# Optimization experiments

Measured on AMD Instinct MI355X. Metric: run time of the kernel, lower is better.

The kernel has to match this reference:

```python
import jax, jax.numpy as jnp
import numpy as np

GRAPH_WEIGHT = 0.3


def setup_inputs() -> dict:
    key = jax.random.key(0)
    ks = jax.random.split(key, 6)
    B, N, NB, MAXKV, BS = 8, 1048576, 8192, 32, 128
    logits = jax.random.normal(ks[0], (B, N, 1), dtype=jnp.float32)
    targets = jax.random.bernoulli(ks[1], 0.5, (B, N)).astype(jnp.float32)
    sup_mask = jax.random.bernoulli(ks[2], 0.1, (B, N))
    ignore_mask = jax.random.bernoulli(ks[3], 0.05, (B, N))
    kv_indices = jax.random.randint(ks[4], (B, NB, MAXKV), 0, NB)
    kv_num_blocks = jax.random.randint(ks[5], (B, NB), 0, MAXKV + 1)
    return {
        "logits": logits,
        "targets": targets,
        "sup_mask": sup_mask,
        "ignore_mask": ignore_mask,
        "kv_indices": kv_indices,
        "kv_num_blocks": kv_num_blocks,
        "block_size": BS,
    }


def _loss(logits, targets, sup_mask, ignore_mask, kv_indices, kv_num_blocks, block_size):
    x = logits.squeeze(-1)                      # [B, N]
    B, N = x.shape
    nb = N // block_size
    dt = x.dtype

    # ---- supervised BCE over sup_mask (== BCEWithLogitsLoss on gathered set) ----
    per = jnp.maximum(x, 0) - x * targets + jnp.log1p(jnp.exp(-jnp.abs(x)))
    supf = sup_mask.astype(dt)
    sup_cnt = supf.sum()
    loss_sup = jnp.where(sup_cnt > 0, (per * supf).sum() / jnp.maximum(sup_cnt, 1), jnp.asarray(0, dt))

    # ---- graph smoothness (block-sparse neighbor-mean squared error) ----
    probs = jax.nn.sigmoid(x)                   # [B, N]
    uncertain = (~ignore_mask) & (~sup_mask)
    keep = (~ignore_mask).astype(dt)

    pblk = probs.reshape(B, nb, block_size)     # [B, nb, BS]
    kblk = keep.reshape(B, nb, block_size)
    block_sum = (pblk * kblk).sum(-1)           # [B, nb] sum of non-ignored probs per block
    block_cnt = kblk.sum(-1)                    # [B, nb]

    max_kv = kv_indices.shape[-1]
    flat_idx = kv_indices.reshape(B, nb * max_kv)
    g_sum = jnp.take_along_axis(block_sum, flat_idx, axis=1).reshape(B, nb, max_kv)
    g_cnt = jnp.take_along_axis(block_cnt, flat_idx, axis=1).reshape(B, nb, max_kv)
    kv_valid = (jnp.arange(max_kv)[None, None, :] < kv_num_blocks[..., None]).astype(dt)
    neigh_sum = (g_sum * kv_valid).sum(-1)      # [B, nb]
    neigh_cnt = (g_cnt * kv_valid).sum(-1)
    neigh_mean = neigh_sum / jnp.maximum(neigh_cnt, 1)

    ublk = uncertain.reshape(B, nb, block_size).astype(dt)
    q_cnt = ublk.sum(-1)                        # [B, nb] uncertain q nodes per block
    valid_block = (q_cnt > 0) & (kv_num_blocks > 0) & (neigh_cnt > 0)

    sq = (((pblk - neigh_mean[..., None]) ** 2) * ublk).sum(-1)  # [B, nb]
    vb = valid_block.astype(dt)
    loss_b = (sq * vb).sum(-1)                  # [B]
    count_b = (q_cnt * vb).sum(-1)              # [B]
    batch_valid = count_b > 0
    per_batch = jnp.where(batch_valid, loss_b / jnp.maximum(count_b, 1), 0.0)
    loss_graph = per_batch.sum() / jnp.maximum(batch_valid.sum(), 1).astype(dt)
    loss_graph = jnp.where(uncertain.any(), loss_graph, jnp.asarray(0, dt))

    return loss_sup + GRAPH_WEIGHT * loss_graph


def reference(logits, targets, sup_mask, ignore_mask, kv_indices, kv_num_blocks, block_size):
    return _loss(logits, targets, sup_mask, ignore_mask, kv_indices, kv_num_blocks, block_size)
```

## Files before the change

kernel.cpp:

```cpp
#include <hip/hip_runtime.h>

constexpr int BATCH = 8;
constexpr int NPB   = 1 << 20;
constexpr int BS    = 128;
constexpr int NB    = NPB / BS;
constexpr int NBLK  = BATCH * NB;
constexpr int MAXKV = 32;

#define GRAPH_WEIGHT 0.3f

constexpr int P1_WGS = (BATCH * NPB) / (256 * 8);
constexpr int P2_WGS = 2048;

constexpr int WS_BSC = 0;
constexpr int WS_QUP = 2 * NBLK;
constexpr int WS_SUP = WS_QUP + 4 * NBLK;
constexpr int WS_P2  = WS_SUP + 2 * P1_WGS;

typedef float v4f __attribute__((ext_vector_type(4)));
typedef int   v4i __attribute__((ext_vector_type(4)));

__global__ __launch_bounds__(256) void k_phase1(const v4f* __restrict__ lg4,
                                                const v4f* __restrict__ tg4,
                                                const v4i* __restrict__ sm4,
                                                const v4i* __restrict__ im4,
                                                float* __restrict__ ws)
{
    const int lane = threadIdx.x & 63;
    const int wid  = (blockIdx.x << 2) + (threadIdx.x >> 6);
    const int grp  = lane >> 4;
    const int sub  = lane & 15;
    const int blk  = (wid << 2) + grp;
    const int c0   = (blk << 5) + sub;

    v4f xv[2], tv[2];
    v4i sv[2], gv[2];
    xv[0] = __builtin_nontemporal_load(lg4 + c0);
    xv[1] = __builtin_nontemporal_load(lg4 + c0 + 16);
    tv[0] = __builtin_nontemporal_load(tg4 + c0);
    tv[1] = __builtin_nontemporal_load(tg4 + c0 + 16);
    sv[0] = __builtin_nontemporal_load(sm4 + c0);
    sv[1] = __builtin_nontemporal_load(sm4 + c0 + 16);
    gv[0] = __builtin_nontemporal_load(im4 + c0);
    gv[1] = __builtin_nontemporal_load(im4 + c0 + 16);

    float sup_sum = 0.f, sup_cnt = 0.f;
    float bsum = 0.f, bcnt = 0.f, q = 0.f, up = 0.f, up2 = 0.f;

#pragma unroll
    for (int j = 0; j < 2; ++j) {
#pragma unroll
        for (int k = 0; k < 4; ++k) {
            const float x = xv[j][k], t = tv[j][k];
            const bool s = (sv[j][k] != 0);
            const bool g = (gv[j][k] != 0);

            const float ax  = fabsf(x);
            const float e   = __expf(-ax);
            const float lp  = __logf(1.f + e);
            const float per = fmaxf(x, 0.f) - x * t + lp;
            const float inv = 1.f / (1.f + e);
            const float p   = (x >= 0.f) ? inv : e * inv;

            if (s) { sup_sum += per; sup_cnt += 1.f; }
            if (!g) { bsum += p; bcnt += 1.f; }
            if (!g && !s) { q += 1.f; up += p; up2 += p * p; }
        }
    }

#pragma unroll
    for (int d = 8; d >= 1; d >>= 1) {
        bsum += __shfl_xor(bsum, d);
        bcnt += __shfl_xor(bcnt, d);
        q    += __shfl_xor(q, d);
        up   += __shfl_xor(up, d);
        up2  += __shfl_xor(up2, d);
    }
    if (sub == 0) {
        *reinterpret_cast<float2*>(ws + WS_BSC + 2 * blk) = make_float2(bsum, bcnt);
        *reinterpret_cast<float4*>(ws + WS_QUP + 4 * blk) = make_float4(q, up, up2, 0.f);
    }

#pragma unroll
    for (int d = 32; d >= 1; d >>= 1) {
        sup_sum += __shfl_xor(sup_sum, d);
        sup_cnt += __shfl_xor(sup_cnt, d);
    }
    __shared__ float lsup[4][2];
    const int w = threadIdx.x >> 6;
    if (lane == 0) { lsup[w][0] = sup_sum; lsup[w][1] = sup_cnt; }
    __syncthreads();
    if (threadIdx.x == 0) {
        const float a = lsup[0][0] + lsup[1][0] + lsup[2][0] + lsup[3][0];
        const float b = lsup[0][1] + lsup[1][1] + lsup[2][1] + lsup[3][1];
        *reinterpret_cast<float2*>(ws + WS_SUP + 2 * blockIdx.x) = make_float2(a, b);
    }
}

__global__ __launch_bounds__(256) void k_phase2(const int* __restrict__ kvi,
                                                const int* __restrict__ kvn,
                                                float* __restrict__ ws)
{
    const int hw     = threadIdx.x >> 5;
    const int lane32 = threadIdx.x & 31;
    const int h0     = blockIdx.x * 32 + hw * 4;
    const int bbase  = (blockIdx.x >> 8) << 13;

    const v4i nkv4 = *reinterpret_cast<const v4i*>(kvn + h0);

    int idxs[4];
#pragma unroll
    for (int j = 0; j < 4; ++j)
        idxs[j] = __builtin_nontemporal_load(kvi + (size_t)(h0 + j) * MAXKV + lane32);

    float gsv[4], gcv[4];
#pragma unroll
    for (int j = 0; j < 4; ++j) {
        float gs = 0.f, gc = 0.f;
        if (lane32 < nkv4[j]) {
            const float2 v = *reinterpret_cast<const float2*>(ws + WS_BSC + 2 * (bbase + idxs[j]));
            gs = v.x; gc = v.y;
        }
#pragma unroll
        for (int d = 16; d >= 1; d >>= 1) {
            gs += __shfl_xor(gs, d);
            gc += __shfl_xor(gc, d);
        }
        gsv[j] = gs; gcv[j] = gc;
    }

    float L = 0.f, C = 0.f, U = 0.f;
    if (lane32 < 4) {
        const int k = lane32;
        const float4 quv = *reinterpret_cast<const float4*>(ws + WS_QUP + 4 * (h0 + k));
        const float q = quv.x, up = quv.y, up2 = quv.z;
        const float gs = gsv[k], gc = gcv[k];
        const float m  = gs / fmaxf(gc, 1.f);
        const bool  vb = (q > 0.f) && (nkv4[k] > 0) && (gc > 0.f);
        const float sq = up2 - 2.f * m * up + m * m * q;
        L = vb ? sq : 0.f;
        C = vb ? q  : 0.f;
        U = q;
    }
#pragma unroll
    for (int d = 2; d >= 1; d >>= 1) {
        L += __shfl_xor(L, d);
        C += __shfl_xor(C, d);
        U += __shfl_xor(U, d);
    }

    __shared__ float l2s[8][3];
    if (lane32 == 0) { l2s[hw][0] = L; l2s[hw][1] = C; l2s[hw][2] = U; }
    __syncthreads();
    if (threadIdx.x == 0) {
        float Ls = 0.f, Cs = 0.f, Us = 0.f;
#pragma unroll
        for (int j = 0; j < 8; ++j) { Ls += l2s[j][0]; Cs += l2s[j][1]; Us += l2s[j][2]; }
        *reinterpret_cast<float4*>(ws + WS_P2 + 4 * blockIdx.x) = make_float4(Ls, Cs, Us, 0.f);
    }
}

__global__ __launch_bounds__(512) void k_phase3(const float* __restrict__ ws,
                                                float* __restrict__ out)
{
    const int tid  = threadIdx.x;
    const int lane = tid & 63;
    const int w    = tid >> 6;

    __shared__ float lsup[8][2];
    __shared__ float lfin[8][3];

    const v4f* supf4 = reinterpret_cast<const v4f*>(ws + WS_SUP);
    float ss = 0.f, sc = 0.f;
#pragma unroll
    for (int j = 0; j < 4; ++j) {
        const v4f v = __builtin_nontemporal_load(supf4 + tid * 4 + j);
        ss += v.x + v.z; sc += v.y + v.w;
    }
#pragma unroll
    for (int d = 32; d >= 1; d >>= 1) { ss += __shfl_xor(ss, d); sc += __shfl_xor(sc, d); }
    if (lane == 0) { lsup[w][0] = ss; lsup[w][1] = sc; }

    const v4f* p2f4 = reinterpret_cast<const v4f*>(ws + WS_P2);
    float L = 0.f, C = 0.f, U = 0.f;
#pragma unroll
    for (int j = 0; j < 4; ++j) {
        const v4f v = __builtin_nontemporal_load(p2f4 + w * 256 + lane * 4 + j);
        L += v.x; C += v.y; U += v.z;
    }
#pragma unroll
    for (int d = 32; d >= 1; d >>= 1) {
        L += __shfl_xor(L, d);
        C += __shfl_xor(C, d);
        U += __shfl_xor(U, d);
    }
    if (lane == 0) { lfin[w][0] = L; lfin[w][1] = C; lfin[w][2] = U; }
    __syncthreads();

    if (tid == 0) {
        float ssum = 0.f, scn = 0.f;
#pragma unroll
        for (int j = 0; j < 8; ++j) { ssum += lsup[j][0]; scn += lsup[j][1]; }
        float per = 0.f, nv = 0.f, uc = 0.f;
#pragma unroll
        for (int b = 0; b < 8; ++b) {
            const float l = lfin[b][0], c = lfin[b][1], u = lfin[b][2];
            if (c > 0.f) { per += l / fmaxf(c, 1.f); nv += 1.f; }
            uc += u;
        }
        const float loss_sup = (scn > 0.f) ? ssum / fmaxf(scn, 1.f) : 0.f;
        float lgr = per / fmaxf(nv, 1.f);
        if (!(uc > 0.f)) lgr = 0.f;
        out[0] = loss_sup + GRAPH_WEIGHT * lgr;
    }
}

extern "C" void kernel_launch(void* const* d_in, const int* in_sizes, int n_in,
                              void* d_out, int out_size, void* d_ws, size_t ws_size,
                              hipStream_t stream) {
    const v4f* lg4 = (const v4f*)d_in[0];
    const v4f* tg4 = (const v4f*)d_in[1];
    const v4i* sm4 = (const v4i*)d_in[2];
    const v4i* im4 = (const v4i*)d_in[3];
    const int* kvi = (const int*)d_in[4];
    const int* kvn = (const int*)d_in[5];
    float* ws  = (float*)d_ws;
    float* out = (float*)d_out;

    k_phase1<<<P1_WGS, 256, 0, stream>>>(lg4, tg4, sm4, im4, ws);
    k_phase2<<<P2_WGS, 256, 0, stream>>>(kvi, kvn, ws);
    k_phase3<<<1, 512, 0, stream>>>(ws, out);
}
```

Before: 164.1 us.

## Fuse final reduction into phase2 via last-block atomic counter; widen phase1 per-thread work

Phase 1 now has each 8-lane group cover one 128-element block, with 16 elements per thread, which halves the workgroup count and shortens the shuffle reduction. The separate single-workgroup phase-3 launch is removed. Phase 2 workgroups instead bump hierarchical atomic counters, and the last one to finish performs the final reduction and writes the output. This saves one kernel launch and its dependency gap, at the cost of atomics and fences, and it relies on phase 1 zeroing the counters before phase 2 runs.

```diff
diff --git a/kernel.cpp b/kernel.cpp
--- a/kernel.cpp
+++ b/kernel.cpp
@@ -9,13 +9,14 @@
 
 #define GRAPH_WEIGHT 0.3f
 
-constexpr int P1_WGS = (BATCH * NPB) / (256 * 8);
+constexpr int P1_WGS = (BATCH * NPB) / (256 * 16);
 constexpr int P2_WGS = 2048;
 
 constexpr int WS_BSC = 0;
 constexpr int WS_QUP = 2 * NBLK;
 constexpr int WS_SUP = WS_QUP + 4 * NBLK;
 constexpr int WS_P2  = WS_SUP + 2 * P1_WGS;
+constexpr int WS_CNT = WS_P2 + 4 * P2_WGS;
 
 typedef float v4f __attribute__((ext_vector_type(4)));
 typedef int   v4i __attribute__((ext_vector_type(4)));
@@ -26,29 +27,32 @@
                                                 const v4i* __restrict__ im4,
                                                 float* __restrict__ ws)
 {
+    if (blockIdx.x == 0 && threadIdx.x < 33)
+        reinterpret_cast<unsigned*>(ws)[WS_CNT + threadIdx.x * 32] = 0u;
+
     const int lane = threadIdx.x & 63;
     const int wid  = (blockIdx.x << 2) + (threadIdx.x >> 6);
-    const int grp  = lane >> 4;
-    const int sub  = lane & 15;
-    const int blk  = (wid << 2) + grp;
+    const int grp  = lane >> 3;
+    const int sub  = lane & 7;
+    const int blk  = (wid << 3) + grp;
     const int c0   = (blk << 5) + sub;
 
-    v4f xv[2], tv[2];
-    v4i sv[2], gv[2];
-    xv[0] = __builtin_nontemporal_load(lg4 + c0);
-    xv[1] = __builtin_nontemporal_load(lg4 + c0 + 16);
-    tv[0] = __builtin_nontemporal_load(tg4 + c0);
-    tv[1] = __builtin_nontemporal_load(tg4 + c0 + 16);
-    sv[0] = __builtin_nontemporal_load(sm4 + c0);
-    sv[1] = __builtin_nontemporal_load(sm4 + c0 + 16);
-    gv[0] = __builtin_nontemporal_load(im4 + c0);
-    gv[1] = __builtin_nontemporal_load(im4 + c0 + 16);
+    v4f xv[4], tv[4];
+    v4i sv[4], gv[4];
+#pragma unroll
+    for (int j = 0; j < 4; ++j) xv[j] = __builtin_nontemporal_load(lg4 + c0 + (j << 3));
+#pragma unroll
+    for (int j = 0; j < 4; ++j) tv[j] = __builtin_nontemporal_load(tg4 + c0 + (j << 3));
+#pragma unroll
+    for (int j = 0; j < 4; ++j) sv[j] = __builtin_nontemporal_load(sm4 + c0 + (j << 3));
+#pragma unroll
+    for (int j = 0; j < 4; ++j) gv[j] = __builtin_nontemporal_load(im4 + c0 + (j << 3));
 
     float sup_sum = 0.f, sup_cnt = 0.f;
     float bsum = 0.f, bcnt = 0.f, q = 0.f, up = 0.f, up2 = 0.f;
 
 #pragma unroll
-    for (int j = 0; j < 2; ++j) {
+    for (int j = 0; j < 4; ++j) {
 #pragma unroll
         for (int k = 0; k < 4; ++k) {
             const float x = xv[j][k], t = tv[j][k];
@@ -69,7 +73,7 @@
     }
 
 #pragma unroll
-    for (int d = 8; d >= 1; d >>= 1) {
+    for (int d = 4; d >= 1; d >>= 1) {
         bsum += __shfl_xor(bsum, d);
         bcnt += __shfl_xor(bcnt, d);
         q    += __shfl_xor(q, d);
@@ -99,10 +103,12 @@
 
 __global__ __launch_bounds__(256) void k_phase2(const int* __restrict__ kvi,
                                                 const int* __restrict__ kvn,
-                                                float* __restrict__ ws)
+                                                float* __restrict__ ws,
+                                                float* __restrict__ out)
 {
-    const int hw     = threadIdx.x >> 5;
-    const int lane32 = threadIdx.x & 31;
+    const int tid    = threadIdx.x;
+    const int hw     = tid >> 5;
+    const int lane32 = tid & 31;
     const int h0     = blockIdx.x * 32 + hw * 4;
     const int bbase  = (blockIdx.x >> 8) << 13;
 
@@ -150,61 +156,74 @@
     }
 
     __shared__ float l2s[8][3];
+    __shared__ bool  is_last;
     if (lane32 == 0) { l2s[hw][0] = L; l2s[hw][1] = C; l2s[hw][2] = U; }
     __syncthreads();
-    if (threadIdx.x == 0) {
+    if (tid == 0) {
         float Ls = 0.f, Cs = 0.f, Us = 0.f;
 #pragma unroll
         for (int j = 0; j < 8; ++j) { Ls += l2s[j][0]; Cs += l2s[j][1]; Us += l2s[j][2]; }
         *reinterpret_cast<float4*>(ws + WS_P2 + 4 * blockIdx.x) = make_float4(Ls, Cs, Us, 0.f);
-    }
-}
-
-__global__ __launch_bounds__(512) void k_phase3(const float* __restrict__ ws,
-                                                float* __restrict__ out)
-{
-    const int tid  = threadIdx.x;
+
+        __threadfence();
+        unsigned* cnts = reinterpret_cast<unsigned*>(ws) + WS_CNT;
+        const unsigned prev = atomicAdd(cnts + (blockIdx.x & 31) * 32, 1u);
+        bool last = false;
+        if (prev == (P2_WGS / 32) - 1) {
+            const unsigned pm = atomicAdd(cnts + 32 * 32, 1u);
+            last = (pm == 31);
+        }
+        is_last = last;
+    }
+    __syncthreads();
+    if (!is_last) return;
+
+    __threadfence();
     const int lane = tid & 63;
     const int w    = tid >> 6;
 
-    __shared__ float lsup[8][2];
-    __shared__ float lfin[8][3];
+    __shared__ float fsup[4][2];
+    __shared__ float ffin[8][3];
 
     const v4f* supf4 = reinterpret_cast<const v4f*>(ws + WS_SUP);
     float ss = 0.f, sc = 0.f;
 #pragma unroll
     for (int j = 0; j < 4; ++j) {
-        const v4f v = __builtin_nontemporal_load(supf4 + tid * 4 + j);
+        const v4f v = supf4[tid * 4 + j];
         ss += v.x + v.z; sc += v.y + v.w;
     }
 #pragma unroll
     for (int d = 32; d >= 1; d >>= 1) { ss += __shfl_xor(ss, d); sc += __shfl_xor(sc, d); }
-    if (lane == 0) { lsup[w][0] = ss; lsup[w][1] = sc; }
+    if (lane == 0) { fsup[w][0] = ss; fsup[w][1] = sc; }
 
     const v4f* p2f4 = reinterpret_cast<const v4f*>(ws + WS_P2);
-    float L = 0.f, C = 0.f, U = 0.f;
-#pragma unroll
-    for (int j = 0; j < 4; ++j) {
-        const v4f v = __builtin_nontemporal_load(p2f4 + w * 256 + lane * 4 + j);
-        L += v.x; C += v.y; U += v.z;
-    }
-#pragma unroll
-    for (int d = 32; d >= 1; d >>= 1) {
-        L += __shfl_xor(L, d);
-        C += __shfl_xor(C, d);
-        U += __shfl_xor(U, d);
-    }
-    if (lane == 0) { lfin[w][0] = L; lfin[w][1] = C; lfin[w][2] = U; }
+#pragma unroll
+    for (int bb = 0; bb < 2; ++bb) {
+        const int b = 2 * w + bb;
+        float Lb = 0.f, Cb = 0.f, Ub = 0.f;
+#pragma unroll
+        for (int j = 0; j < 4; ++j) {
+            const v4f v = p2f4[b * 256 + lane * 4 + j];
+            Lb += v.x; Cb += v.y; Ub += v.z;
+        }
+#pragma unroll
+        for (int d = 32; d >= 1; d >>= 1) {
+            Lb += __shfl_xor(Lb, d);
+            Cb += __shfl_xor(Cb, d);
+            Ub += __shfl_xor(Ub, d);
+        }
+        if (lane == 0) { ffin[b][0] = Lb; ffin[b][1] = Cb; ffin[b][2] = Ub; }
+    }
     __syncthreads();
 
     if (tid == 0) {
         float ssum = 0.f, scn = 0.f;
 #pragma unroll
-        for (int j = 0; j < 8; ++j) { ssum += lsup[j][0]; scn += lsup[j][1]; }
+        for (int j = 0; j < 4; ++j) { ssum += fsup[j][0]; scn += fsup[j][1]; }
         float per = 0.f, nv = 0.f, uc = 0.f;
 #pragma unroll
         for (int b = 0; b < 8; ++b) {
-            const float l = lfin[b][0], c = lfin[b][1], u = lfin[b][2];
+            const float l = ffin[b][0], c = ffin[b][1], u = ffin[b][2];
             if (c > 0.f) { per += l / fmaxf(c, 1.f); nv += 1.f; }
             uc += u;
         }
@@ -228,6 +247,5 @@
     float* out = (float*)d_out;
 
     k_phase1<<<P1_WGS, 256, 0, stream>>>(lg4, tg4, sm4, im4, ws);
-    k_phase2<<<P2_WGS, 256, 0, stream>>>(kvi, kvn, ws);
-    k_phase3<<<1, 512, 0, stream>>>(ws, out);
+    k_phase2<<<P2_WGS, 256, 0, stream>>>(kvi, kvn, ws, out);
 }
```

Measured after the change: 196.7 us. +19.9%, slower.

## Make phase1 persistent with double-buffered loads over eight iterations per wave

Applied to the files above, without the earlier changes.

Phase1 drops from 4096 single-shot workgroups to 512 workgroups, each wave looping over eight groups of four blocks. The loads for the next iteration are issued before computing the current one, so memory latency overlaps with math. This cuts launch and tail overhead and reduces the number of partial sup sums phase3 must read. It also doubles register use for the buffers, which can lower occupancy, and 512 workgroups may not fully saturate HBM bandwidth.

```diff
diff --git a/kernel.cpp b/kernel.cpp
--- a/kernel.cpp
+++ b/kernel.cpp
@@ -9,8 +9,9 @@
 
 #define GRAPH_WEIGHT 0.3f
 
-constexpr int P1_WGS = (BATCH * NPB) / (256 * 8);
-constexpr int P2_WGS = 2048;
+constexpr int P1_WGS   = 512;
+constexpr int P1_ITERS = 8;
+constexpr int P2_WGS   = 2048;
 
 constexpr int WS_BSC = 0;
 constexpr int WS_QUP = 2 * NBLK;
@@ -27,58 +28,70 @@
                                                 float* __restrict__ ws)
 {
     const int lane = threadIdx.x & 63;
-    const int wid  = (blockIdx.x << 2) + (threadIdx.x >> 6);
+    const int wv   = threadIdx.x >> 6;
+    const int W    = (blockIdx.x << 2) + wv;
     const int grp  = lane >> 4;
     const int sub  = lane & 15;
-    const int blk  = (wid << 2) + grp;
-    const int c0   = (blk << 5) + sub;
-
-    v4f xv[2], tv[2];
-    v4i sv[2], gv[2];
-    xv[0] = __builtin_nontemporal_load(lg4 + c0);
-    xv[1] = __builtin_nontemporal_load(lg4 + c0 + 16);
-    tv[0] = __builtin_nontemporal_load(tg4 + c0);
-    tv[1] = __builtin_nontemporal_load(tg4 + c0 + 16);
-    sv[0] = __builtin_nontemporal_load(sm4 + c0);
-    sv[1] = __builtin_nontemporal_load(sm4 + c0 + 16);
-    gv[0] = __builtin_nontemporal_load(im4 + c0);
-    gv[1] = __builtin_nontemporal_load(im4 + c0 + 16);
+    const int cb   = (W * 32 + grp) * 32 + sub;
+
+    v4f xb[2][2], tb[2][2];
+    v4i sb[2][2], gb[2][2];
+
+    auto load_iter = [&](int buf, int it) {
+        const int c = cb + it * 128;
+        xb[buf][0] = __builtin_nontemporal_load(lg4 + c);
+        xb[buf][1] = __builtin_nontemporal_load(lg4 + c + 16);
+        tb[buf][0] = __builtin_nontemporal_load(tg4 + c);
+        tb[buf][1] = __builtin_nontemporal_load(tg4 + c + 16);
+        sb[buf][0] = __builtin_nontemporal_load(sm4 + c);
+        sb[buf][1] = __builtin_nontemporal_load(sm4 + c + 16);
+        gb[buf][0] = __builtin_nontemporal_load(im4 + c);
+        gb[buf][1] = __builtin_nontemporal_load(im4 + c + 16);
+    };
 
     float sup_sum = 0.f, sup_cnt = 0.f;
-    float bsum = 0.f, bcnt = 0.f, q = 0.f, up = 0.f, up2 = 0.f;
-
-#pragma unroll
-    for (int j = 0; j < 2; ++j) {
-#pragma unroll
-        for (int k = 0; k < 4; ++k) {
-            const float x = xv[j][k], t = tv[j][k];
-            const bool s = (sv[j][k] != 0);
-            const bool g = (gv[j][k] != 0);
-
-            const float ax  = fabsf(x);
-            const float e   = __expf(-ax);
-            const float lp  = __logf(1.f + e);
-            const float per = fmaxf(x, 0.f) - x * t + lp;
-            const float inv = 1.f / (1.f + e);
-            const float p   = (x >= 0.f) ? inv : e * inv;
-
-            if (s) { sup_sum += per; sup_cnt += 1.f; }
-            if (!g) { bsum += p; bcnt += 1.f; }
-            if (!g && !s) { q += 1.f; up += p; up2 += p * p; }
-        }
-    }
-
-#pragma unroll
-    for (int d = 8; d >= 1; d >>= 1) {
-        bsum += __shfl_xor(bsum, d);
-        bcnt += __shfl_xor(bcnt, d);
-        q    += __shfl_xor(q, d);
-        up   += __shfl_xor(up, d);
-        up2  += __shfl_xor(up2, d);
-    }
-    if (sub == 0) {
-        *reinterpret_cast<float2*>(ws + WS_BSC + 2 * blk) = make_float2(bsum, bcnt);
-        *reinterpret_cast<float4*>(ws + WS_QUP + 4 * blk) = make_float4(q, up, up2, 0.f);
+    load_iter(0, 0);
+
+#pragma unroll
+    for (int it = 0; it < P1_ITERS; ++it) {
+        if (it + 1 < P1_ITERS) load_iter((it + 1) & 1, it + 1);
+        const int buf = it & 1;
+
+        float bsum = 0.f, bcnt = 0.f, q = 0.f, up = 0.f, up2 = 0.f;
+#pragma unroll
+        for (int h = 0; h < 2; ++h) {
+#pragma unroll
+            for (int k = 0; k < 4; ++k) {
+                const float x = xb[buf][h][k], t = tb[buf][h][k];
+                const bool s = (sb[buf][h][k] != 0);
+                const bool g = (gb[buf][h][k] != 0);
+
+                const float ax  = fabsf(x);
+                const float e   = __expf(-ax);
+                const float lp  = __logf(1.f + e);
+                const float per = fmaxf(x, 0.f) - x * t + lp;
+                const float inv = 1.f / (1.f + e);
+                const float p   = (x >= 0.f) ? inv : e * inv;
+
+                if (s) { sup_sum += per; sup_cnt += 1.f; }
+                if (!g) { bsum += p; bcnt += 1.f; }
+                if (!g && !s) { q += 1.f; up += p; up2 += p * p; }
+            }
+        }
+
+#pragma unroll
+        for (int d = 8; d >= 1; d >>= 1) {
+            bsum += __shfl_xor(bsum, d);
+            bcnt += __shfl_xor(bcnt, d);
+            q    += __shfl_xor(q, d);
+            up   += __shfl_xor(up, d);
+            up2  += __shfl_xor(up2, d);
+        }
+        if (sub == 0) {
+            const int blk = W * 32 + it * 4 + grp;
+            *reinterpret_cast<float2*>(ws + WS_BSC + 2 * blk) = make_float2(bsum, bcnt);
+            *reinterpret_cast<float4*>(ws + WS_QUP + 4 * blk) = make_float4(q, up, up2, 0.f);
+        }
     }
 
 #pragma unroll
@@ -87,8 +100,7 @@
         sup_cnt += __shfl_xor(sup_cnt, d);
     }
     __shared__ float lsup[4][2];
-    const int w = threadIdx.x >> 6;
-    if (lane == 0) { lsup[w][0] = sup_sum; lsup[w][1] = sup_cnt; }
+    if (lane == 0) { lsup[wv][0] = sup_sum; lsup[wv][1] = sup_cnt; }
     __syncthreads();
     if (threadIdx.x == 0) {
         const float a = lsup[0][0] + lsup[1][0] + lsup[2][0] + lsup[3][0];
@@ -172,10 +184,9 @@
 
     const v4f* supf4 = reinterpret_cast<const v4f*>(ws + WS_SUP);
     float ss = 0.f, sc = 0.f;
-#pragma unroll
-    for (int j = 0; j < 4; ++j) {
-        const v4f v = __builtin_nontemporal_load(supf4 + tid * 4 + j);
-        ss += v.x + v.z; sc += v.y + v.w;
+    if (tid < 256) {
+        const v4f v = supf4[tid];
+        ss = v.x + v.z; sc = v.y + v.w;
     }
 #pragma unroll
     for (int d = 32; d >= 1; d >>= 1) { ss += __shfl_xor(ss, d); sc += __shfl_xor(sc, d); }
@@ -185,7 +196,7 @@
     float L = 0.f, C = 0.f, U = 0.f;
 #pragma unroll
     for (int j = 0; j < 4; ++j) {
-        const v4f v = __builtin_nontemporal_load(p2f4 + w * 256 + lane * 4 + j);
+        const v4f v = p2f4[w * 256 + lane * 4 + j];
         L += v.x; C += v.y; U += v.z;
     }
 #pragma unroll
```

Measured after the change: 170.6 us. 1.04x slower.
